# Kernel tuning notes

Hardware: AMD Instinct MI355X
Metric: run time of the kernel (lower is better)

Reference implementation:

```python
import jax, jax.numpy as jnp
import numpy as np

EPS = 1e-5

def _bn(y, g, b):
    # BatchNorm1d training-mode math: biased batch stats over (batch, spatial)
    m = jnp.mean(y, axis=(0, 2), keepdims=True)
    v = jnp.var(y, axis=(0, 2), keepdims=True)
    return (y - m) / jnp.sqrt(v + EPS) * g[None, :, None] + b[None, :, None]

def setup_inputs() -> dict:
    key = jax.random.key(0)
    ks = jax.random.split(key, 8)
    B, C, HW = 32, 512, 1024
    D = C // 8
    s = 0.02
    return {
        "x": jax.random.normal(ks[0], (B, C, HW), dtype=jnp.float32),
        "bn1_g": jnp.ones((C,), jnp.float32),
        "bn1_b": jnp.zeros((C,), jnp.float32),
        "W_qkv": jax.random.normal(ks[1], (2 * D + C, C), jnp.float32) * s,
        "b_qkv": jnp.zeros((2 * D + C,), jnp.float32),
        "bn2_g": jnp.ones((C,), jnp.float32),
        "bn2_b": jnp.zeros((C,), jnp.float32),
        "W1": jax.random.normal(ks[2], (C, C), jnp.float32) * s,
        "b1": jnp.zeros((C,), jnp.float32),
        "W2": jax.random.normal(ks[3], (C, C), jnp.float32) * s,
        "b2": jnp.zeros((C,), jnp.float32),
    }

def reference(x, bn1_g, bn1_b, W_qkv, b_qkv, bn2_g, bn2_b, W1, b1, W2, b2):
    b, c, hw = x.shape
    d = c // 8
    h = jax.nn.relu(_bn(x, bn1_g, bn1_b))
    # 1x1 conv == channel matmul: [b, 2d+c, hw]
    qkv = jnp.einsum('oc,bch->boh', W_qkv, h) + b_qkv[None, :, None]
    q, k, v = qkv[:, :d], qkv[:, d:2 * d], qkv[:, 2 * d:]
    # beta[b, q_pos, k_pos]; note softmax over axis=1 (query axis), per original
    beta = jnp.einsum('bdq,bdk->bqk', q, k) / jnp.sqrt(jnp.asarray(d, x.dtype))
    beta = jax.nn.softmax(beta, axis=1)
    att = jnp.einsum('bcq,bqk->bck', v, beta)  # [b, c, hw]
    xr = x + att
    y = _bn(xr, bn2_g, bn2_b)
    y = jnp.transpose(y, (0, 2, 1))  # [b, hw, c]
    y = jax.nn.relu(y @ W1.T + b1) @ W2.T + b2
    return xr + jnp.transpose(y, (0, 2, 1))
```

## Files before the change

kernel.cpp:

```cpp
#include <hip/hip_runtime.h>

#define BB 32
#define CC 512
#define HWN 1024
#define DD 64
#define OO 640

typedef short bf16x8 __attribute__((ext_vector_type(8)));
typedef float f32x4 __attribute__((ext_vector_type(4)));
typedef __attribute__((address_space(1))) const void gvoid;
typedef __attribute__((address_space(3))) void svoid;

__device__ __forceinline__ void gload_lds16(const void* g, void* l) {
    __builtin_amdgcn_global_load_lds((gvoid*)g, (svoid*)l, 16, 0, 0);
}

__device__ __forceinline__ unsigned short f2bf(float f) {
    unsigned int u = __float_as_uint(f);
    unsigned int r = u + 0x7FFFu + ((u >> 16) & 1u);
    return (unsigned short)(r >> 16);
}
__device__ __forceinline__ float bf2f(unsigned short h) {
    return __uint_as_float(((unsigned int)h) << 16);
}

__global__ __launch_bounds__(256) void cvt3_kernel(const float* __restrict__ a,
                                                   const float* __restrict__ b,
                                                   const float* __restrict__ c,
                                                   unsigned short* __restrict__ oa,
                                                   unsigned short* __restrict__ ob,
                                                   unsigned short* __restrict__ oc) {
    const int n1 = OO * CC, n2 = CC * CC;
    int i = blockIdx.x * 256 + threadIdx.x;
    if (i < n1)            oa[i] = f2bf(a[i]);
    else if (i < n1 + n2)  ob[i - n1] = f2bf(b[i - n1]);
    else                   oc[i - n1 - n2] = f2bf(c[i - n1 - n2]);
}

template <bool INBF16>
__global__ __launch_bounds__(256) void bn_stats_kernel(const void* __restrict__ xv,
                                                       float* __restrict__ mean,
                                                       float* __restrict__ rstd) {
    int c = blockIdx.x;
    int t = threadIdx.x;
    float s = 0.f, s2 = 0.f;
    if (INBF16) {
        const unsigned int* x = (const unsigned int*)xv;
        for (int b = 0; b < BB; ++b) {
            const unsigned int* p = x + ((size_t)b * CC + c) * (HWN / 2);
#pragma unroll
            for (int i = 0; i < 2; ++i) {
                unsigned int w = p[t + i * 256];
                float v0 = bf2f((unsigned short)(w & 0xffffu));
                float v1 = bf2f((unsigned short)(w >> 16));
                s += v0 + v1; s2 += v0 * v0 + v1 * v1;
            }
        }
    } else {
        const float* x = (const float*)xv;
        for (int b = 0; b < BB; ++b) {
            const float* p = x + ((size_t)b * CC + c) * HWN;
#pragma unroll
            for (int i = 0; i < 4; ++i) {
                float v = p[t + i * 256];
                s += v; s2 += v * v;
            }
        }
    }
    for (int off = 32; off > 0; off >>= 1) {
        s  += __shfl_down(s,  off, 64);
        s2 += __shfl_down(s2, off, 64);
    }
    __shared__ float sh[4], sh2[4];
    int wave = t >> 6;
    if ((t & 63) == 0) { sh[wave] = s; sh2[wave] = s2; }
    __syncthreads();
    if (t == 0) {
        float ts = 0.f, ts2 = 0.f;
        for (int w = 0; w < 4; ++w) { ts += sh[w]; ts2 += sh2[w]; }
        const float invN = 1.f / (float)(BB * HWN);
        float m = ts * invN;
        float var = ts2 * invN - m * m;
        mean[c] = m;
        rstd[c] = rsqrtf(var + 1e-5f);
    }
}

template <bool RELU, bool INBF16>
__global__ __launch_bounds__(256) void bn_apply_t_kernel(const void* __restrict__ xv,
                                                         const float* __restrict__ mean,
                                                         const float* __restrict__ rstd,
                                                         const float* __restrict__ g,
                                                         const float* __restrict__ bta,
                                                         unsigned short* __restrict__ outT) {
    __shared__ float tile[64][65];
    int b  = blockIdx.z;
    int c0 = blockIdx.y * 64;
    int s0 = blockIdx.x * 64;
    int t = threadIdx.x;
    int sl = t & 63, grp = t >> 6;
#pragma unroll
    for (int i = 0; i < 16; ++i) {
        int cr = i * 4 + grp;
        int c = c0 + cr;
        float r  = rstd[c] * g[c];
        float sh = bta[c] - mean[c] * r;
        float xval;
        if (INBF16) {
            const unsigned short* xb = (const unsigned short*)xv;
            xval = bf2f(xb[((size_t)b * CC + c0 + cr) * HWN + s0 + sl]);
        } else {
            const float* xb = (const float*)xv;
            xval = xb[((size_t)b * CC + c0 + cr) * HWN + s0 + sl];
        }
        float v = fmaf(xval, r, sh);
        if (RELU) v = fmaxf(v, 0.f);
        tile[cr][sl] = v;
    }
    __syncthreads();
    unsigned short* ob = outT + ((size_t)b * HWN + s0) * CC + c0;
#pragma unroll
    for (int i = 0; i < 16; ++i) {
        int srow = i * 4 + grp;
        ob[(size_t)srow * CC + sl] = f2bf(tile[sl][srow]);
    }
}

__global__ __launch_bounds__(256) void reduce_bnstats_kernel(const float* __restrict__ part,
                                                             float* __restrict__ mean,
                                                             float* __restrict__ rstd) {
    int c = blockIdx.x * 256 + threadIdx.x;
    float s = 0.f, s2 = 0.f;
    for (int p = 0; p < BB * 8; ++p) {
        s  += part[(size_t)p * 1024 + c];
        s2 += part[(size_t)p * 1024 + 512 + c];
    }
    const float invN = 1.f / (float)(BB * HWN);
    float m = s * invN;
    mean[c] = m;
    rstd[c] = rsqrtf(s2 * invN - m * m + 1e-5f);
}

__global__ __launch_bounds__(512, 4) void fused_pv_kernel(
        const unsigned short* __restrict__ qkTg,
        const unsigned short* __restrict__ vg,
        const float* __restrict__ xg,
        unsigned short* __restrict__ xrg,
        float* __restrict__ rowpart) {
    __shared__ __align__(16) unsigned short Ks[2 * 128 * 32];
    __shared__ __align__(16) unsigned short Qs[2 * 64 * 32];
    __shared__ __align__(16) unsigned short Vs[2 * 256 * 32];
    __shared__ __align__(16) unsigned short Es[2 * 128 * 32];
    __shared__ float sS[128];
    __shared__ float rsS[2][256];
    __shared__ float rqS[2][256];

    int lin = blockIdx.x + 16 * blockIdx.z;
    int b  = lin & 31;
    int nn = (lin >> 5) & 7;
    int ch = lin >> 8;
    int n0 = nn * 128;
    int c0 = ch * 256;
    const unsigned short* qk = qkTg + (size_t)b * (HWN * 128);
    const unsigned short* vb = vg + (size_t)b * ((size_t)CC * HWN);
    int t = threadIdx.x;
    int wv = t >> 6, L = t & 63;
    int lr = L & 15, lq = L >> 4;
    int swz = (lr >> 1) & 3;
    int cstrip = (wv >> 1) * 64;
    int khalf = (wv & 1) * 64;

#pragma unroll
    for (int is = 0; is < 2; ++is) {
        int idx = is * 512 + t;
        int kkd = idx >> 9, row = (idx >> 2) & 127, slot = idx & 3;
        int chk = slot ^ ((row >> 1) & 3);
        gload_lds16(qk + (size_t)(n0 + row) * 128 + 64 + kkd * 32 + chk * 8, &Ks[idx * 8]);
    }
    {
        int kkd = t >> 8, row = (t >> 2) & 63, slot = t & 3;
        int chk = slot ^ ((row >> 1) & 3);
        gload_lds16(qk + (size_t)row * 128 + kkd * 32 + chk * 8, &Qs[t * 8]);
    }

    f32x4 acc[4][4] = {};
    float S = 0.f;
    for (int i = 0; i < 16; ++i) {
        int q0 = i * 64;
#pragma unroll
        for (int is = 0; is < 4; ++is) {
            int idx = is * 512 + t;
            int kkq = idx >> 10, row = (idx >> 2) & 255, slot = idx & 3;
            int chk = slot ^ ((row >> 1) & 3);
            gload_lds16(vb + (size_t)(c0 + row) * HWN + q0 + kkq * 32 + chk * 8, &Vs[idx * 8]);
        }
        if (i == 0) __syncthreads();

        f32x4 eacc[4] = {};
#pragma unroll
        for (int kkd = 0; kkd < 2; ++kkd) {
            bf16x8 kb = *(const bf16x8*)&Ks[kkd * 4096 + (wv * 16 + lr) * 32 + ((lq ^ swz) * 8)];
#pragma unroll
            for (int qi = 0; qi < 4; ++qi) {
                bf16x8 qa = *(const bf16x8*)&Qs[kkd * 2048 + (qi * 16 + lr) * 32 + ((lq ^ swz) * 8)];
                eacc[qi] = __builtin_amdgcn_mfma_f32_16x16x32_bf16(qa, kb, eacc[qi], 0, 0, 0);
            }
        }
        float spart = 0.f;
#pragma unroll
        for (int qi = 0; qi < 4; ++qi) {
            float e0 = __expf(eacc[qi][0] * 0.125f);
            float e1 = __expf(eacc[qi][1] * 0.125f);
            float e2 = __expf(eacc[qi][2] * 0.125f);
            float e3 = __expf(eacc[qi][3] * 0.125f);
            spart += (e0 + e1) + (e2 + e3);
            unsigned int lo = (unsigned int)f2bf(e0) | ((unsigned int)f2bf(e1) << 16);
            unsigned int hi = (unsigned int)f2bf(e2) | ((unsigned int)f2bf(e3) << 16);
            int kkq = qi >> 1;
            int chunkE = (qi & 1) * 2 + (lq >> 1);
            int addr = kkq * 4096 + (wv * 16 + lr) * 32 + ((chunkE ^ swz) * 8) + (lq & 1) * 4;
            *(uint2*)&Es[addr] = make_uint2(lo, hi);
        }
        spart += __shfl_xor(spart, 16, 64);
        spart += __shfl_xor(spart, 32, 64);
        S += spart;
        __syncthreads();

        if (i + 1 < 16) {
            int kkd = t >> 8, row = (t >> 2) & 63, slot = t & 3;
            int chk = slot ^ ((row >> 1) & 3);
            gload_lds16(qk + (size_t)(q0 + 64 + row) * 128 + kkd * 32 + chk * 8, &Qs[t * 8]);
        }

#pragma unroll
        for (int kk = 0; kk < 2; ++kk) {
            bf16x8 af[4], bfj[4];
#pragma unroll
            for (int ii = 0; ii < 4; ++ii)
                af[ii] = *(const bf16x8*)&Vs[kk * 8192 + (cstrip + ii * 16 + lr) * 32 + ((lq ^ swz) * 8)];
#pragma unroll
            for (int j = 0; j < 4; ++j)
                bfj[j] = *(const bf16x8*)&Es[kk * 4096 + (khalf + j * 16 + lr) * 32 + ((lq ^ swz) * 8)];
#pragma unroll
            for (int ii = 0; ii < 4; ++ii)
#pragma unroll
                for (int j = 0; j < 4; ++j)
                    acc[ii][j] = __builtin_amdgcn_mfma_f32_16x16x32_bf16(af[ii], bfj[j], acc[ii][j], 0, 0, 0);
        }
        __syncthreads();
    }

    if (lq == 0) sS[wv * 16 + lr] = S;
    __syncthreads();
    float inv[4];
#pragma unroll
    for (int j = 0; j < 4; ++j) inv[j] = 1.f / sS[khalf + j * 16 + lr];

    const float* xb = xg + (size_t)b * ((size_t)CC * HWN);
    unsigned short* xrb = xrg + (size_t)b * ((size_t)CC * HWN);
#pragma unroll
    for (int ii = 0; ii < 4; ++ii) {
#pragma unroll
        for (int r = 0; r < 4; ++r) {
            int rloc = cstrip + ii * 16 + lq * 4 + r;
            int row = c0 + rloc;
            float s = 0.f, q2 = 0.f;
#pragma unroll
            for (int j = 0; j < 4; ++j) {
                int col = n0 + khalf + j * 16 + lr;
                float val = acc[ii][j][r] * inv[j];
                size_t off = (size_t)row * HWN + col;
                val += xb[off];
                s += val; q2 += val * val;
                xrb[off] = f2bf(val);
            }
#pragma unroll
            for (int m = 1; m <= 8; m <<= 1) {
                s += __shfl_xor(s, m, 64);
                q2 += __shfl_xor(q2, m, 64);
            }
            if (lr == 0) { rsS[wv & 1][rloc] = s; rqS[wv & 1][rloc] = q2; }
        }
    }
    __syncthreads();
    {
        size_t base = ((size_t)b * 8 + nn) * 1024;
        int rloc = t & 255;
        if (t < 256) rowpart[base + c0 + rloc]       = rsS[0][rloc] + rsS[1][rloc];
        else         rowpart[base + 512 + c0 + rloc] = rqS[0][rloc] + rqS[1][rloc];
    }
}

template <bool OUTBF16, int BIASMODE , bool RELU,
          int RESMODE >
__global__ __launch_bounds__(256, 4) void mfma_gemm(const unsigned short* __restrict__ A,
                                                 const unsigned short* __restrict__ Bt,
                                                 const float* __restrict__ bias,
                                                 const void* __restrict__ resid,
                                                 void* __restrict__ C,
                                                 int K, int lda, int ldb, int ldc,
                                                 long strideA, long strideB, long strideC,
                                                 float scale) {
    __shared__ __align__(16) unsigned short As[2][128 * 32];
    __shared__ __align__(16) unsigned short Bs[2][128 * 32];
    int b  = blockIdx.z;
    int m0 = blockIdx.y * 128;
    int n0 = blockIdx.x * 128;
    const unsigned short* Ab = A  + (size_t)b * strideA;
    const unsigned short* Bb = Bt + (size_t)b * strideB;
    int t = threadIdx.x;
    int wv = t >> 6, L = t & 63;
    int wm = (wv >> 1) * 64, wn = (wv & 1) * 64;
    int lr = L & 15, lq = L >> 4;
    int srow = t >> 2;
    int gchunk = (t & 3) ^ ((t >> 3) & 3);
    int skof = gchunk * 8;
    int swz = (lr >> 1) & 3;

    int aoff[4], boff[4];
#pragma unroll
    for (int i = 0; i < 4; ++i) {
        aoff[i] = (wm + i * 16 + lr) * 32 + ((lq ^ swz) * 8);
        boff[i] = (wn + i * 16 + lr) * 32 + ((lq ^ swz) * 8);
    }

    const unsigned short* gA0 = Ab + (size_t)(m0 + srow) * lda + skof;
    const unsigned short* gA1 = Ab + (size_t)(m0 + 64 + srow) * lda + skof;
    const unsigned short* gB0 = Bb + (size_t)(n0 + srow) * ldb + skof;
    const unsigned short* gB1 = Bb + (size_t)(n0 + 64 + srow) * ldb + skof;

    f32x4 acc[4][4] = {};
    int nIter = K >> 5;

    gload_lds16(gA0, &As[0][t * 8]);
    gload_lds16(gA1, &As[0][64 * 32 + t * 8]);
    gload_lds16(gB0, &Bs[0][t * 8]);
    gload_lds16(gB1, &Bs[0][64 * 32 + t * 8]);

    int p = 0;
    for (int i = 0; i < nIter; ++i) {
        __syncthreads();
        if (i + 1 < nIter) {
            int ko = (i + 1) << 5;
            gload_lds16(gA0 + ko, &As[p ^ 1][t * 8]);
            gload_lds16(gA1 + ko, &As[p ^ 1][64 * 32 + t * 8]);
            gload_lds16(gB0 + ko, &Bs[p ^ 1][t * 8]);
            gload_lds16(gB1 + ko, &Bs[p ^ 1][64 * 32 + t * 8]);
        }
        bf16x8 af[4], bfr[4];
#pragma unroll
        for (int j = 0; j < 4; ++j) af[j]  = *(const bf16x8*)&As[p][aoff[j]];
#pragma unroll
        for (int j = 0; j < 4; ++j) bfr[j] = *(const bf16x8*)&Bs[p][boff[j]];
#pragma unroll
        for (int ii = 0; ii < 4; ++ii)
#pragma unroll
            for (int jj = 0; jj < 4; ++jj)
                acc[ii][jj] = __builtin_amdgcn_mfma_f32_16x16x32_bf16(af[ii], bfr[jj], acc[ii][jj], 0, 0, 0);
        p ^= 1;
    }

#pragma unroll
    for (int i = 0; i < 4; ++i) {
#pragma unroll
        for (int r = 0; r < 4; ++r) {
            int row = m0 + wm + i * 16 + lq * 4 + r;
            float brow = (BIASMODE == 1) ? bias[row] : 0.f;
#pragma unroll
            for (int j = 0; j < 4; ++j) {
                int col = n0 + wn + j * 16 + lr;
                float v = acc[i][j][r] * scale;
                if (BIASMODE == 1) v += brow;
                if (BIASMODE == 2) v += bias[col];
                if (RELU) v = fmaxf(v, 0.f);
                size_t off = (size_t)b * strideC + (size_t)row * ldc + col;
                if (RESMODE == 1) v += ((const float*)resid)[off];
                if (RESMODE == 2) v += bf2f(((const unsigned short*)resid)[off]);
                if (OUTBF16) ((unsigned short*)C)[off] = f2bf(v);
                else         ((float*)C)[off] = v;
            }
        }
    }
}

extern "C" void kernel_launch(void* const* d_in, const int* in_sizes, int n_in,
                              void* d_out, int out_size, void* d_ws, size_t ws_size,
                              hipStream_t stream) {
    const float* x     = (const float*)d_in[0];
    const float* bn1_g = (const float*)d_in[1];
    const float* bn1_b = (const float*)d_in[2];
    const float* W_qkv = (const float*)d_in[3];
    const float* b_qkv = (const float*)d_in[4];
    const float* bn2_g = (const float*)d_in[5];
    const float* bn2_b = (const float*)d_in[6];
    const float* W1    = (const float*)d_in[7];
    const float* b1    = (const float*)d_in[8];
    const float* W2    = (const float*)d_in[9];
    const float* b2    = (const float*)d_in[10];
    float* out = (float*)d_out;
    char* ws = (char*)d_ws;

    unsigned short* hT    = (unsigned short*)(ws);
    unsigned short* qkT   = (unsigned short*)(ws + 33554432);
    unsigned short* v     = (unsigned short*)(ws + 41943040);
    unsigned short* xr    = (unsigned short*)(ws + 142606336);
    unsigned short* Wqkvb = (unsigned short*)(ws + 176160768);
    unsigned short* W1b   = (unsigned short*)(ws + 176816128);
    unsigned short* W2b   = (unsigned short*)(ws + 177340416);
    float* stats = (float*)(ws + 177864704);
    float* mean1 = stats,        *rstd1 = stats + 512;
    float* mean2 = stats + 1024, *rstd2 = stats + 1536;
    unsigned short* ybnT = hT;
    unsigned short* y1T  = v;
    float* rowpartBN = (float*)(ws + 1179648);

    const long sHT = (long)HWN * CC;
    const long sQK = (long)HWN * 128;
    const long sV  = (long)CC * HWN;

    cvt3_kernel<<<(OO * CC + 2 * CC * CC) / 256, 256, 0, stream>>>(W_qkv, W1, W2, Wqkvb, W1b, W2b);
    bn_stats_kernel<false><<<CC, 256, 0, stream>>>(x, mean1, rstd1);
    bn_apply_t_kernel<true, false><<<dim3(16, 8, BB), 256, 0, stream>>>(x, mean1, rstd1, bn1_g, bn1_b, hT);
    mfma_gemm<true, 2, false, 0><<<dim3(1, 8, BB), 256, 0, stream>>>(
        hT, Wqkvb, b_qkv, nullptr, qkT, 512, 512, 512, 128, sHT, 0, sQK, 1.f);
    mfma_gemm<true, 1, false, 0><<<dim3(8, 4, BB), 256, 0, stream>>>(
        Wqkvb + 128 * 512, hT, b_qkv + 128, nullptr, v, 512, 512, 512, 1024, 0, sHT, sV, 1.f);
    fused_pv_kernel<<<dim3(16, 1, BB), 512, 0, stream>>>(qkT, v, x, xr, rowpartBN);
    reduce_bnstats_kernel<<<2, 256, 0, stream>>>(rowpartBN, mean2, rstd2);
    bn_apply_t_kernel<false, true><<<dim3(16, 8, BB), 256, 0, stream>>>(xr, mean2, rstd2, bn2_g, bn2_b, ybnT);
    mfma_gemm<true, 2, true, 0><<<dim3(4, 8, BB), 256, 0, stream>>>(
        ybnT, W1b, b1, nullptr, y1T, 512, 512, 512, 512, sHT, 0, sHT, 1.f);
    mfma_gemm<false, 1, false, 2><<<dim3(8, 4, BB), 256, 0, stream>>>(
        W2b, y1T, b2, xr, out, 512, 512, 512, 1024, 0, sHT, sV, 1.f);
}
```

Before: 366.4 us.

## Double-buffer V tiles and load Q/K fragments directly from global

Restructures the fused PV attention kernel: V tiles are now double-buffered in LDS, with the next tile prefetched while the current one is consumed. K fragments are held in registers for the whole loop and Q fragments are read straight from global memory, which removes the Ks/Qs LDS buffers. The mid-loop barrier becomes a raw s_barrier waiting only on lgkmcnt, and the reduction scratch arrays alias the E buffer. The aim is to hide global load latency behind MFMA work, though the direct global Q reads in the inner loop may expose latency, and the LDS footprint grows with the doubled V buffer.

```diff
diff --git a/kernel.cpp b/kernel.cpp
--- a/kernel.cpp
+++ b/kernel.cpp
@@ -147,13 +147,11 @@
         const float* __restrict__ xg,
         unsigned short* __restrict__ xrg,
         float* __restrict__ rowpart) {
-    __shared__ __align__(16) unsigned short Ks[2 * 128 * 32];
-    __shared__ __align__(16) unsigned short Qs[2 * 64 * 32];
-    __shared__ __align__(16) unsigned short Vs[2 * 256 * 32];
+    __shared__ __align__(16) unsigned short Vs[2][2 * 256 * 32];
     __shared__ __align__(16) unsigned short Es[2 * 128 * 32];
-    __shared__ float sS[128];
-    __shared__ float rsS[2][256];
-    __shared__ float rqS[2][256];
+    float* sS  = (float*)Es;
+    float* rsS = (float*)Es + 128;
+    float* rqS = (float*)Es + 128 + 512;
 
     int lin = blockIdx.x + 16 * blockIdx.z;
     int b  = lin & 31;
@@ -170,40 +168,43 @@
     int cstrip = (wv >> 1) * 64;
     int khalf = (wv & 1) * 64;
 
-#pragma unroll
-    for (int is = 0; is < 2; ++is) {
+    bf16x8 kfr[2];
+#pragma unroll
+    for (int kkd = 0; kkd < 2; ++kkd)
+        kfr[kkd] = *(const bf16x8*)(qk + (size_t)(n0 + wv * 16 + lr) * 128 + 64 + kkd * 32 + lq * 8);
+
+#pragma unroll
+    for (int is = 0; is < 4; ++is) {
         int idx = is * 512 + t;
-        int kkd = idx >> 9, row = (idx >> 2) & 127, slot = idx & 3;
+        int kkq = idx >> 10, row = (idx >> 2) & 255, slot = idx & 3;
         int chk = slot ^ ((row >> 1) & 3);
-        gload_lds16(qk + (size_t)(n0 + row) * 128 + 64 + kkd * 32 + chk * 8, &Ks[idx * 8]);
-    }
-    {
-        int kkd = t >> 8, row = (t >> 2) & 63, slot = t & 3;
-        int chk = slot ^ ((row >> 1) & 3);
-        gload_lds16(qk + (size_t)row * 128 + kkd * 32 + chk * 8, &Qs[t * 8]);
-    }
+        gload_lds16(vb + (size_t)(c0 + row) * HWN + kkq * 32 + chk * 8, &Vs[0][idx * 8]);
+    }
+    __syncthreads();
 
     f32x4 acc[4][4] = {};
     float S = 0.f;
+    int p = 0;
     for (int i = 0; i < 16; ++i) {
         int q0 = i * 64;
-#pragma unroll
-        for (int is = 0; is < 4; ++is) {
-            int idx = is * 512 + t;
-            int kkq = idx >> 10, row = (idx >> 2) & 255, slot = idx & 3;
-            int chk = slot ^ ((row >> 1) & 3);
-            gload_lds16(vb + (size_t)(c0 + row) * HWN + q0 + kkq * 32 + chk * 8, &Vs[idx * 8]);
-        }
-        if (i == 0) __syncthreads();
+        if (i + 1 < 16) {
+#pragma unroll
+            for (int is = 0; is < 4; ++is) {
+                int idx = is * 512 + t;
+                int kkq = idx >> 10, row = (idx >> 2) & 255, slot = idx & 3;
+                int chk = slot ^ ((row >> 1) & 3);
+                gload_lds16(vb + (size_t)(c0 + row) * HWN + q0 + 64 + kkq * 32 + chk * 8,
+                            &Vs[p ^ 1][idx * 8]);
+            }
+        }
 
         f32x4 eacc[4] = {};
 #pragma unroll
         for (int kkd = 0; kkd < 2; ++kkd) {
-            bf16x8 kb = *(const bf16x8*)&Ks[kkd * 4096 + (wv * 16 + lr) * 32 + ((lq ^ swz) * 8)];
 #pragma unroll
             for (int qi = 0; qi < 4; ++qi) {
-                bf16x8 qa = *(const bf16x8*)&Qs[kkd * 2048 + (qi * 16 + lr) * 32 + ((lq ^ swz) * 8)];
-                eacc[qi] = __builtin_amdgcn_mfma_f32_16x16x32_bf16(qa, kb, eacc[qi], 0, 0, 0);
+                bf16x8 qa = *(const bf16x8*)(qk + (size_t)(q0 + qi * 16 + lr) * 128 + kkd * 32 + lq * 8);
+                eacc[qi] = __builtin_amdgcn_mfma_f32_16x16x32_bf16(qa, kfr[kkd], eacc[qi], 0, 0, 0);
             }
         }
         float spart = 0.f;
@@ -224,20 +225,18 @@
         spart += __shfl_xor(spart, 16, 64);
         spart += __shfl_xor(spart, 32, 64);
         S += spart;
-        __syncthreads();
-
-        if (i + 1 < 16) {
-            int kkd = t >> 8, row = (t >> 2) & 63, slot = t & 3;
-            int chk = slot ^ ((row >> 1) & 3);
-            gload_lds16(qk + (size_t)(q0 + 64 + row) * 128 + kkd * 32 + chk * 8, &Qs[t * 8]);
-        }
+
+        __builtin_amdgcn_sched_barrier(0);
+        asm volatile("s_waitcnt lgkmcnt(0)" ::: "memory");
+        __builtin_amdgcn_s_barrier();
+        __builtin_amdgcn_sched_barrier(0);
 
 #pragma unroll
         for (int kk = 0; kk < 2; ++kk) {
             bf16x8 af[4], bfj[4];
 #pragma unroll
             for (int ii = 0; ii < 4; ++ii)
-                af[ii] = *(const bf16x8*)&Vs[kk * 8192 + (cstrip + ii * 16 + lr) * 32 + ((lq ^ swz) * 8)];
+                af[ii] = *(const bf16x8*)&Vs[p][kk * 8192 + (cstrip + ii * 16 + lr) * 32 + ((lq ^ swz) * 8)];
 #pragma unroll
             for (int j = 0; j < 4; ++j)
                 bfj[j] = *(const bf16x8*)&Es[kk * 4096 + (khalf + j * 16 + lr) * 32 + ((lq ^ swz) * 8)];
@@ -248,6 +247,7 @@
                     acc[ii][j] = __builtin_amdgcn_mfma_f32_16x16x32_bf16(af[ii], bfj[j], acc[ii][j], 0, 0, 0);
         }
         __syncthreads();
+        p ^= 1;
     }
 
     if (lq == 0) sS[wv * 16 + lr] = S;
@@ -279,15 +279,15 @@
                 s += __shfl_xor(s, m, 64);
                 q2 += __shfl_xor(q2, m, 64);
             }
-            if (lr == 0) { rsS[wv & 1][rloc] = s; rqS[wv & 1][rloc] = q2; }
+            if (lr == 0) { rsS[(wv & 1) * 256 + rloc] = s; rqS[(wv & 1) * 256 + rloc] = q2; }
         }
     }
     __syncthreads();
     {
         size_t base = ((size_t)b * 8 + nn) * 1024;
         int rloc = t & 255;
-        if (t < 256) rowpart[base + c0 + rloc]       = rsS[0][rloc] + rsS[1][rloc];
-        else         rowpart[base + 512 + c0 + rloc] = rqS[0][rloc] + rqS[1][rloc];
+        if (t < 256) rowpart[base + c0 + rloc]       = rsS[rloc] + rsS[256 + rloc];
+        else         rowpart[base + 512 + c0 + rloc] = rqS[rloc] + rqS[256 + rloc];
     }
 }
 
```

After: 387.2 us. 1.06x slower.
